# Kernel optimization log

Measured on AMD Instinct MI355X. Metric: run time of the kernel, lower is better.

The kernel has to match this reference:

```python
import jax, jax.numpy as jnp
import numpy as np

B, R, N, K, E = 128, 500, 500, 10, 128
H1 = 5 * E  # UnvisitedMLP hidden = embedding_dim * 5


def setup_inputs() -> dict:
    key = jax.random.key(0)
    ks = jax.random.split(key, 8)
    current = jax.random.randint(ks[0], (B, R), 0, N)
    distance = jax.random.uniform(ks[1], (B, N, N), dtype=jnp.float32)
    # unvisited cities, exercising the padding-index path in search_unvisited.
    visited = jax.random.uniform(ks[2], (B, R, N)) < 0.97
    masked = jnp.where(visited, -jnp.inf, 0.0).astype(jnp.float32)
    encoded_nodes = jax.random.normal(ks[3], (B, N, E), dtype=jnp.float32)
    w1 = jax.random.normal(ks[4], (H1, K * E), dtype=jnp.float32) * (1.0 / np.sqrt(K * E))
    b1 = jnp.zeros((H1,), dtype=jnp.float32)
    w2 = jax.random.normal(ks[5], (E, H1), dtype=jnp.float32) * (1.0 / np.sqrt(H1))
    b2 = jnp.zeros((E,), dtype=jnp.float32)
    return {"current": current, "distance": distance, "masked": masked,
            "encoded_nodes": encoded_nodes, "w1": w1, "b1": b1, "w2": w2, "b2": b2}


def _search_unvisited(current, distance, masked, k_near):
    # distance_filtered[b, r, :] = distance[b, current[b, r], :]  -> [B, R, N]
    b_idx = jnp.arange(current.shape[0])[:, None]
    distance_filtered = distance[b_idx, current, :]
    mask_unvisited = masked != -jnp.inf
    distance_masked = jnp.where(mask_unvisited, distance_filtered, jnp.inf)
    # k smallest == top-k of negated distances
    neg_vals, k_idx = jax.lax.top_k(-distance_masked, k_near)  # [B, R, K]
    is_inf = neg_vals == -jnp.inf  # entries that were +inf (no unvisited left)
    n_cities = distance.shape[1]
    return jnp.where(is_inf, n_cities, k_idx)  # padding index = problem_size


def _gather_pad0(encoded_nodes, idx):
    # pad encoded_nodes with a zero row at index N, then gather  -> [B, R, K, E]
    padded = jnp.concatenate(
        [encoded_nodes, jnp.zeros_like(encoded_nodes[:, :1, :])], axis=1)
    b_idx = jnp.arange(encoded_nodes.shape[0])[:, None, None]
    return padded[b_idx, idx, :]


def _pad_avg(a):
    # replace all-zero (padding) rows along K with the mean of non-zero rows
    is_zero = a.sum(axis=-1) == 0  # [B, R, K]
    nz_count = jnp.clip((~is_zero).sum(axis=-1).astype(jnp.float32), 1e-9)
    mean_vec = a.sum(axis=2) / nz_count[..., None]  # [B, R, E]
    return jnp.where(is_zero[..., None], mean_vec[:, :, None, :], a)


def reference(current, distance, masked, encoded_nodes, w1, b1, w2, b2):
    k_near = K
    idx = _search_unvisited(current, distance, masked, k_near)  # [B, R, K]
    emb = _gather_pad0(encoded_nodes, idx)                      # [B, R, K, E]
    emb = _pad_avg(emb)
    h = emb.reshape(emb.shape[0], emb.shape[1], k_near * emb.shape[-1])  # [B, R, K*E]
    h = jax.nn.relu(jnp.einsum('brf,hf->brh', h, w1) + b1)
    out = jnp.einsum('brh,eh->bre', h, w2) + b2  # [B, R, E]
    return out
```

## Files before the change

kernel.cpp:

```cpp
#include <hip/hip_runtime.h>
#include <cstdint>
#include <cstddef>

#define Bn   128
#define Rn   500
#define Nn   500
#define Kn   10
#define En   128
#define H1n  640
#define KEn  1280
#define Mn   (Bn * Rn)

typedef short s16x8 __attribute__((ext_vector_type(8)));
typedef float f32x4 __attribute__((ext_vector_type(4)));

__device__ __forceinline__ unsigned short f2bf(float x) {
    union { float f; unsigned int u; } v; v.f = x;
    unsigned int r = v.u + 0x7fffu + ((v.u >> 16) & 1u);
    return (unsigned short)(r >> 16);
}
__device__ __forceinline__ float bf2f(unsigned short u) {
    union { unsigned int u; float f; } v; v.u = ((unsigned int)u) << 16;
    return v.f;
}
__device__ __forceinline__ void gl2lds16(const void* g, void* l) {
    __builtin_amdgcn_global_load_lds(
        (const __attribute__((address_space(1))) unsigned int*)g,
        (__attribute__((address_space(3))) unsigned int*)l, 16, 0, 0);
}
__device__ __forceinline__ void drain_all() {
    asm volatile("s_waitcnt vmcnt(0) lgkmcnt(0)" ::: "memory");
}
#define WAITV(n) asm volatile("s_waitcnt vmcnt(" #n ")" ::: "memory")
__device__ __forceinline__ void pipe_barrier() {
    __builtin_amdgcn_s_barrier();
    asm volatile("" ::: "memory");
}

__global__ void convw_kernel(const float* __restrict__ enc, const float* __restrict__ w1,
                             const float* __restrict__ w2,
                             unsigned short* __restrict__ encb, unsigned short* __restrict__ w1b,
                             unsigned short* __restrict__ w2b) {
    int i = blockIdx.x * 256 + threadIdx.x;
    if (i < (Bn * Nn * En) / 4) {
        float4 v = ((const float4*)enc)[i];
        ushort4 o; o.x = f2bf(v.x); o.y = f2bf(v.y); o.z = f2bf(v.z); o.w = f2bf(v.w);
        ((ushort4*)encb)[i] = o;
    }
    if (i < (H1n * KEn) / 4) {
        float4 v = ((const float4*)w1)[i];
        ushort4 o; o.x = f2bf(v.x); o.y = f2bf(v.y); o.z = f2bf(v.z); o.w = f2bf(v.w);
        ((ushort4*)w1b)[i] = o;
    }
    if (i < (En * H1n) / 4) {
        float4 v = ((const float4*)w2)[i];
        ushort4 o; o.x = f2bf(v.x); o.y = f2bf(v.y); o.z = f2bf(v.z); o.w = f2bf(v.w);
        ((ushort4*)w2b)[i] = o;
    }
}

__global__ __launch_bounds__(256) void select_kernel(const int* __restrict__ current,
                            const float* __restrict__ distance,
                            const float* __restrict__ masked,
                            const unsigned short* __restrict__ encb,
                            int* __restrict__ idx_out,
                            unsigned short* __restrict__ meanbb) {
    __shared__ unsigned long long buf[4][512];
    const int wv   = threadIdx.x >> 6;
    const int row  = blockIdx.x * 4 + wv;
    const int lane = threadIdx.x & 63;
    const int b    = row / Rn;
    const int cur  = current[row];
    const uint4* drow4 = (const uint4*)(distance + ((size_t)b * Nn + cur) * Nn);
    const uint4* mrow4 = (const uint4*)(masked + (size_t)row * Nn);
    unsigned long long* wbuf = buf[wv];
    const unsigned long long INFKEY = 0x7F800000FFFFFFFFull;

    uint4 mu[2], du[2];
#pragma unroll
    for (int h = 0; h < 2; ++h) {
        const int c = lane + 64 * h;
        mu[h] = make_uint4(0xFF800000u, 0xFF800000u, 0xFF800000u, 0xFF800000u);
        du[h] = make_uint4(0u, 0u, 0u, 0u);
        if (c < 125) { mu[h] = mrow4[c]; du[h] = drow4[c]; }
    }

    unsigned long long keyr[8];
    unsigned int fm = 0;
#pragma unroll
    for (int h = 0; h < 2; ++h) {
        const unsigned int mm[4] = {mu[h].x, mu[h].y, mu[h].z, mu[h].w};
        const unsigned int dd[4] = {du[h].x, du[h].y, du[h].z, du[h].w};
#pragma unroll
        for (int j = 0; j < 4; ++j) {
            const int e  = h * 4 + j;
            const int nn = 4 * (lane + 64 * h) + j;
            keyr[e] = ((unsigned long long)dd[j] << 32) | (unsigned int)nn;
            fm |= (mm[j] != 0xFF800000u ? 1u : 0u) << e;
        }
    }
    const int lc = __popc(fm);

    int x = lc;
#pragma unroll
    for (int d = 1; d < 64; d <<= 1) {
        const int y = __shfl_up(x, d);
        if (lane >= d) x += y;
    }
    const int n = __shfl(x, 63);
    int off = x - lc;

#pragma unroll
    for (int e = 0; e < 8; ++e) {
        if (fm & (1u << e)) wbuf[off++] = keyr[e];
    }

    int ids[Kn];
    if (n <= 64) {
        unsigned long long key = (lane < n) ? wbuf[lane] : INFKEY;
#pragma unroll
        for (int k = 2; k <= 32; k <<= 1) {
#pragma unroll
            for (int j = k >> 1; j >= 1; j >>= 1) {
                const unsigned long long ok = __shfl_xor(key, j);
                const bool takemin = (((lane & k) == 0) == ((lane & j) == 0));
                const unsigned long long mn = (ok < key) ? ok : key;
                const unsigned long long mx = (ok < key) ? key : ok;
                key = takemin ? mn : mx;
            }
        }
        if (n > 32) {
#pragma unroll
            for (int j = 32; j >= 1; j >>= 1) {
                const unsigned long long ok = __shfl_xor(key, j);
                const bool takemin = (((lane & 64) == 0) == ((lane & j) == 0));
                const unsigned long long mn = (ok < key) ? ok : key;
                const unsigned long long mx = (ok < key) ? key : ok;
                key = takemin ? mn : mx;
            }
        }
        const int wid = ((unsigned int)(key >> 32) >= 0x7F800000u) ? Nn
                                                                   : (int)(key & 0xffffffffu);
        if (lane < Kn) idx_out[row * Kn + lane] = wid;
#pragma unroll
        for (int k = 0; k < Kn; ++k) ids[k] = __shfl(wid, k);
    } else {
        unsigned long long key8[8];
#pragma unroll
        for (int i = 0; i < 8; ++i) {
            const int ii = lane + 64 * i;
            key8[i] = (ii < n) ? wbuf[ii] : INFKEY;
        }
        int myid = Nn;
#pragma unroll
        for (int it = 0; it < Kn; ++it) {
            unsigned long long bk = key8[0];
#pragma unroll
            for (int i = 1; i < 8; ++i) bk = (key8[i] < bk) ? key8[i] : bk;
#pragma unroll
            for (int off2 = 1; off2 < 64; off2 <<= 1) {
                const unsigned long long ok = __shfl_xor(bk, off2);
                bk = (ok < bk) ? ok : bk;
            }
            const int wid = ((unsigned int)(bk >> 32) >= 0x7F800000u) ? Nn
                                                                      : (int)(bk & 0xffffffffu);
            ids[it] = wid;
            if (lane == it) myid = wid;
#pragma unroll
            for (int i = 0; i < 8; ++i)
                if (key8[i] == bk) key8[i] = INFKEY;
        }
        if (lane < Kn) idx_out[row * Kn + lane] = myid;
    }

    const unsigned int* encu = (const unsigned int*)(encb + (size_t)b * Nn * En);
    float s0 = 0.f, s1 = 0.f; int cnt = 0;
#pragma unroll
    for (int k = 0; k < Kn; ++k) {
        const int id = ids[k];
        if (id < Nn) {
            unsigned int u = encu[id * (En / 2) + lane];
            s0 += bf2f((unsigned short)(u & 0xffffu));
            s1 += bf2f((unsigned short)(u >> 16));
            cnt++;
        }
    }
    float m0 = 0.f, m1 = 0.f;
    if (cnt > 0) { m0 = s0 / (float)cnt; m1 = s1 / (float)cnt; }
    unsigned int packed = (unsigned int)f2bf(m0) | ((unsigned int)f2bf(m1) << 16);
    ((unsigned int*)meanbb)[(size_t)row * (En / 2) + lane] = packed;
}

__global__ __launch_bounds__(512, 4) void gemm1_kernel(
        const unsigned short* __restrict__ encb, const unsigned short* __restrict__ meanbb,
        const int* __restrict__ idxb, const unsigned short* __restrict__ w1b,
        const float* __restrict__ b1, unsigned short* __restrict__ hbuf) {
    extern __shared__ unsigned short lds[];
    unsigned short* const As   = lds;
    unsigned short* const Bs   = lds + 3 * 256 * 32;
    unsigned short* const idxs = lds + 3 * 256 * 32 + 3 * 128 * 32;

    const int p  = blockIdx.x;
    const int x  = p & 7;
    const int rk = p >> 3;
    const int w  = (x < 2 ? x * 157 : 314 + (x - 2) * 156) + rk;
    const int row0 = (w / 5) * 256;
    const int h0   = (w % 5) * 128;

    const int t    = threadIdx.x;
    const int lane = t & 63;
    const int wave = t >> 6;
    const int ln15 = lane & 15;
    const int q4   = lane >> 4;
    const int wm4  = wave & 3;
    const int wn   = wave >> 2;

    for (int i = t; i < 256 * Kn; i += 512)
        idxs[i] = (unsigned short)idxb[row0 * Kn + i];

    const int rl   = lane >> 2;
    const int sc   = lane & 3;
    const int coff = (sc ^ ((rl >> 1) & 3)) * 8;

    int lrowA[2];
    const unsigned short* encB[2];
    const unsigned short* meanR[2];
#pragma unroll
    for (int s = 0; s < 2; ++s) {
        lrowA[s] = wave * 32 + s * 16 + rl;
        const int gr = row0 + lrowA[s];
        encB[s]  = encb + (size_t)(gr / Rn) * Nn * En;
        meanR[s] = meanbb + (size_t)gr * En + coff;
    }
    const int lrowB = wave * 16 + rl;
    const unsigned short* w1R = w1b + (size_t)(h0 + lrowB) * KEn + coff;

    f32x4 acc[4][4];
#pragma unroll
    for (int i = 0; i < 4; ++i)
#pragma unroll
        for (int j = 0; j < 4; ++j)
            acc[i][j] = (f32x4){0.f, 0.f, 0.f, 0.f};

    auto issueA = [&](int kt, int cb) {
        const int j  = kt >> 2;
        const int e0 = (kt & 3) * 32;
#pragma unroll
        for (int s = 0; s < 2; ++s) {
            const int id = idxs[lrowA[s] * Kn + j];
            const unsigned short* src = (id < Nn)
                ? (encB[s] + (size_t)id * En + e0 + coff)
                : (meanR[s] + e0);
            gl2lds16(src, As + (size_t)cb * (256 * 32) + (wave * 32 + s * 16) * 32);
        }
    };
    auto issueB = [&](int kt, int cb) {
        gl2lds16(w1R + kt * 32, Bs + (size_t)cb * (128 * 32) + (wave * 16) * 32);
    };

    drain_all();
    __syncthreads();
    issueA(0, 0); issueB(0, 0);
    issueA(1, 1); issueB(1, 1);
    WAITV(3);
    pipe_barrier();

    const int rA  = wm4 * 64 + ln15;
    const int rB  = wn  * 64 + ln15;
    const int slA = (q4 ^ ((rA >> 1) & 3)) * 8;
    const int slB = (q4 ^ ((rB >> 1) & 3)) * 8;

#define MFMA16(a, bvec, c) c = __builtin_amdgcn_mfma_f32_16x16x32_bf16(a, bvec, c, 0, 0, 0)

#pragma unroll
    for (int kt = 0; kt < 40; ++kt) {
        const int cb = kt % 3;
        const unsigned short* Ab = As + cb * (256 * 32);
        const unsigned short* Bb = Bs + cb * (128 * 32);
        s16x8 af0, af1, af2, af3, bq0, bq1;

        af0 = *(const s16x8*)(Ab + (rA +  0) * 32 + slA);
        af1 = *(const s16x8*)(Ab + (rA + 16) * 32 + slA);
        af2 = *(const s16x8*)(Ab + (rA + 32) * 32 + slA);
        af3 = *(const s16x8*)(Ab + (rA + 48) * 32 + slA);
        bq0 = *(const s16x8*)(Bb + (rB +  0) * 32 + slB);
        bq1 = *(const s16x8*)(Bb + (rB + 16) * 32 + slB);
        if (kt + 2 < 40) issueA(kt + 2, (kt + 2) % 3);
        pipe_barrier();
        __builtin_amdgcn_s_setprio(1);
        MFMA16(af0, bq0, acc[0][0]); MFMA16(af1, bq0, acc[1][0]);
        MFMA16(af2, bq0, acc[2][0]); MFMA16(af3, bq0, acc[3][0]);
        MFMA16(af0, bq1, acc[0][1]); MFMA16(af1, bq1, acc[1][1]);
        MFMA16(af2, bq1, acc[2][1]); MFMA16(af3, bq1, acc[3][1]);
        __builtin_amdgcn_s_setprio(0);
        pipe_barrier();

        bq0 = *(const s16x8*)(Bb + (rB + 32) * 32 + slB);
        bq1 = *(const s16x8*)(Bb + (rB + 48) * 32 + slB);
        if (kt + 2 < 40) issueB(kt + 2, (kt + 2) % 3);
        pipe_barrier();
        __builtin_amdgcn_s_setprio(1);
        MFMA16(af0, bq0, acc[0][2]); MFMA16(af1, bq0, acc[1][2]);
        MFMA16(af2, bq0, acc[2][2]); MFMA16(af3, bq0, acc[3][2]);
        MFMA16(af0, bq1, acc[0][3]); MFMA16(af1, bq1, acc[1][3]);
        MFMA16(af2, bq1, acc[2][3]); MFMA16(af3, bq1, acc[3][3]);
        __builtin_amdgcn_s_setprio(0);
        if (kt + 2 < 40)      { WAITV(3); }
        else if (kt + 1 < 40) { WAITV(0); }
        pipe_barrier();
    }
#undef MFMA16

#pragma unroll
    for (int i = 0; i < 4; ++i) {
#pragma unroll
        for (int jj = 0; jj < 4; ++jj) {
            const int h = h0 + wn * 64 + jj * 16 + ln15;
            const float bias = b1[h];
#pragma unroll
            for (int rg = 0; rg < 4; ++rg) {
                const int m = wm4 * 64 + i * 16 + q4 * 4 + rg;
                float vv = acc[i][jj][rg] + bias;
                vv = fmaxf(vv, 0.f);
                hbuf[(size_t)(row0 + m) * H1n + h] = f2bf(vv);
            }
        }
    }
}

__global__ __launch_bounds__(256, 4) void gemm2_kernel(
        const unsigned short* __restrict__ hbuf, const unsigned short* __restrict__ w2b,
        const float* __restrict__ b2, float* __restrict__ out) {
    __shared__ alignas(16) unsigned short As[3][128 * 32];
    __shared__ alignas(16) unsigned short Bs[3][128 * 32];

    const int row0 = blockIdx.x * 128;
    const int t    = threadIdx.x;
    const int lane = t & 63;
    const int wave = t >> 6;
    const int ln15 = lane & 15;
    const int q4   = lane >> 4;
    const int wm   = wave & 1;
    const int wn   = wave >> 1;

    const int rl   = lane >> 2;
    const int sc   = lane & 3;
    const int coff = (sc ^ ((rl >> 1) & 3)) * 8;

    const unsigned short* hrow[2];
    const unsigned short* w2row[2];
#pragma unroll
    for (int s = 0; s < 2; ++s) {
        const int lr = wave * 32 + s * 16 + rl;
        hrow[s]  = hbuf + (size_t)(row0 + lr) * H1n + coff;
        w2row[s] = w2b + (size_t)lr * H1n + coff;
    }

    f32x4 acc[4][4];
#pragma unroll
    for (int i = 0; i < 4; ++i)
#pragma unroll
        for (int j = 0; j < 4; ++j)
            acc[i][j] = (f32x4){0.f, 0.f, 0.f, 0.f};

    auto issueA = [&](int kt, int cb) {
#pragma unroll
        for (int s = 0; s < 2; ++s)
            gl2lds16(hrow[s] + kt * 32, &As[cb][(wave * 32 + s * 16) * 32]);
    };
    auto issueB = [&](int kt, int cb) {
#pragma unroll
        for (int s = 0; s < 2; ++s)
            gl2lds16(w2row[s] + kt * 32, &Bs[cb][(wave * 32 + s * 16) * 32]);
    };

    issueA(0, 0); issueB(0, 0);
    issueA(1, 1); issueB(1, 1);
    WAITV(4);
    pipe_barrier();

    const int rA  = wm * 64 + ln15;
    const int rB  = wn * 64 + ln15;
    const int slA = (q4 ^ ((rA >> 1) & 3)) * 8;
    const int slB = (q4 ^ ((rB >> 1) & 3)) * 8;

#define MFMA16(a, bvec, c) c = __builtin_amdgcn_mfma_f32_16x16x32_bf16(a, bvec, c, 0, 0, 0)

#pragma unroll
    for (int kt = 0; kt < 20; ++kt) {
        const int cb = kt % 3;
        const unsigned short* Ab = As[cb];
        const unsigned short* Bb = Bs[cb];
        s16x8 af0, af1, af2, af3, bq0, bq1;

        af0 = *(const s16x8*)(Ab + (rA +  0) * 32 + slA);
        af1 = *(const s16x8*)(Ab + (rA + 16) * 32 + slA);
        af2 = *(const s16x8*)(Ab + (rA + 32) * 32 + slA);
        af3 = *(const s16x8*)(Ab + (rA + 48) * 32 + slA);
        bq0 = *(const s16x8*)(Bb + (rB +  0) * 32 + slB);
        bq1 = *(const s16x8*)(Bb + (rB + 16) * 32 + slB);
        if (kt + 2 < 20) issueA(kt + 2, (kt + 2) % 3);
        pipe_barrier();
        __builtin_amdgcn_s_setprio(1);
        MFMA16(af0, bq0, acc[0][0]); MFMA16(af1, bq0, acc[1][0]);
        MFMA16(af2, bq0, acc[2][0]); MFMA16(af3, bq0, acc[3][0]);
        MFMA16(af0, bq1, acc[0][1]); MFMA16(af1, bq1, acc[1][1]);
        MFMA16(af2, bq1, acc[2][1]); MFMA16(af3, bq1, acc[3][1]);
        __builtin_amdgcn_s_setprio(0);
        pipe_barrier();

        bq0 = *(const s16x8*)(Bb + (rB + 32) * 32 + slB);
        bq1 = *(const s16x8*)(Bb + (rB + 48) * 32 + slB);
        if (kt + 2 < 20) issueB(kt + 2, (kt + 2) % 3);
        pipe_barrier();
        __builtin_amdgcn_s_setprio(1);
        MFMA16(af0, bq0, acc[0][2]); MFMA16(af1, bq0, acc[1][2]);
        MFMA16(af2, bq0, acc[2][2]); MFMA16(af3, bq0, acc[3][2]);
        MFMA16(af0, bq1, acc[0][3]); MFMA16(af1, bq1, acc[1][3]);
        MFMA16(af2, bq1, acc[2][3]); MFMA16(af3, bq1, acc[3][3]);
        __builtin_amdgcn_s_setprio(0);
        if (kt + 2 < 20)      { WAITV(4); }
        else if (kt + 1 < 20) { WAITV(0); }
        pipe_barrier();
    }
#undef MFMA16

#pragma unroll
    for (int i = 0; i < 4; ++i) {
#pragma unroll
        for (int jj = 0; jj < 4; ++jj) {
            const int e = wn * 64 + jj * 16 + ln15;
            const float bias = b2[e];
#pragma unroll
            for (int rg = 0; rg < 4; ++rg) {
                const int m = wm * 64 + i * 16 + q4 * 4 + rg;
                out[(size_t)(row0 + m) * En + e] = acc[i][jj][rg] + bias;
            }
        }
    }
}

extern "C" void kernel_launch(void* const* d_in, const int* in_sizes, int n_in,
                              void* d_out, int out_size, void* d_ws, size_t ws_size,
                              hipStream_t stream) {
    const int*   current  = (const int*)d_in[0];
    const float* distance = (const float*)d_in[1];
    const float* masked   = (const float*)d_in[2];
    const float* encoded  = (const float*)d_in[3];
    const float* w1       = (const float*)d_in[4];
    const float* b1       = (const float*)d_in[5];
    const float* w2       = (const float*)d_in[6];
    const float* b2       = (const float*)d_in[7];
    float* out = (float*)d_out;

    char* ws = (char*)d_ws;
    const size_t OFF_IDX  = 0;
    const size_t OFF_ENCB = 2560000;
    const size_t OFF_MEAN = OFF_ENCB + 16384000;
    const size_t OFF_W1B  = OFF_MEAN + 16384000;
    const size_t OFF_W2B  = OFF_W1B + 1638400;
    const size_t OFF_H    = OFF_W2B + 163840;
    int*            idxb   = (int*)(ws + OFF_IDX);
    unsigned short* encb   = (unsigned short*)(ws + OFF_ENCB);
    unsigned short* meanbb = (unsigned short*)(ws + OFF_MEAN);
    unsigned short* w1b    = (unsigned short*)(ws + OFF_W1B);
    unsigned short* w2b    = (unsigned short*)(ws + OFF_W2B);
    unsigned short* hbuf   = (unsigned short*)(ws + OFF_H);

    static bool s_attr = false;
    if (!s_attr) {
        hipFuncSetAttribute(reinterpret_cast<const void*>(gemm1_kernel),
                            hipFuncAttributeMaxDynamicSharedMemorySize, 78848);
        s_attr = true;
    }

    convw_kernel<<<(Bn * Nn * En / 4 + 255) / 256, 256, 0, stream>>>(encoded, w1, w2, encb, w1b, w2b);
    select_kernel<<<Mn / 4, 256, 0, stream>>>(current, distance, masked, encb, idxb, meanbb);
    gemm1_kernel<<<1250, 512, 78848, stream>>>(encb, meanbb, idxb, w1b, b1, hbuf);
    gemm2_kernel<<<Mn / 128, 256, 0, stream>>>(hbuf, w2b, b2, out);
}
```

Before: 439.5 us.

## Process four rows per wave in select with prefetch; merge gemm2 k-step phases

The select kernel now has each wave handle four consecutive rows. The next row's distance and mask loads are double-buffered so they overlap the current row's sort and mean work, and the grid shrinks by four. Separately, the gemm2 inner loop loads all four B fragments up front, issues both the A and B async copies together, and runs all 16 MFMAs in a single phase. That drops two pipe barriers per k-step, at the cost of more registers and fewer waves in flight in select.

```diff
diff --git a/kernel.cpp b/kernel.cpp
--- a/kernel.cpp
+++ b/kernel.cpp
@@ -66,129 +66,146 @@
                             int* __restrict__ idx_out,
                             unsigned short* __restrict__ meanbb) {
     __shared__ unsigned long long buf[4][512];
-    const int wv   = threadIdx.x >> 6;
-    const int row  = blockIdx.x * 4 + wv;
-    const int lane = threadIdx.x & 63;
-    const int b    = row / Rn;
-    const int cur  = current[row];
-    const uint4* drow4 = (const uint4*)(distance + ((size_t)b * Nn + cur) * Nn);
-    const uint4* mrow4 = (const uint4*)(masked + (size_t)row * Nn);
+    const int wv    = threadIdx.x >> 6;
+    const int lane  = threadIdx.x & 63;
+    const int rbase = blockIdx.x * 16 + wv * 4;
     unsigned long long* wbuf = buf[wv];
     const unsigned long long INFKEY = 0x7F800000FFFFFFFFull;
 
-    uint4 mu[2], du[2];
-#pragma unroll
-    for (int h = 0; h < 2; ++h) {
-        const int c = lane + 64 * h;
-        mu[h] = make_uint4(0xFF800000u, 0xFF800000u, 0xFF800000u, 0xFF800000u);
-        du[h] = make_uint4(0u, 0u, 0u, 0u);
-        if (c < 125) { mu[h] = mrow4[c]; du[h] = drow4[c]; }
-    }
-
-    unsigned long long keyr[8];
-    unsigned int fm = 0;
-#pragma unroll
-    for (int h = 0; h < 2; ++h) {
-        const unsigned int mm[4] = {mu[h].x, mu[h].y, mu[h].z, mu[h].w};
-        const unsigned int dd[4] = {du[h].x, du[h].y, du[h].z, du[h].w};
-#pragma unroll
-        for (int j = 0; j < 4; ++j) {
-            const int e  = h * 4 + j;
-            const int nn = 4 * (lane + 64 * h) + j;
-            keyr[e] = ((unsigned long long)dd[j] << 32) | (unsigned int)nn;
-            fm |= (mm[j] != 0xFF800000u ? 1u : 0u) << e;
-        }
-    }
-    const int lc = __popc(fm);
-
-    int x = lc;
-#pragma unroll
-    for (int d = 1; d < 64; d <<= 1) {
-        const int y = __shfl_up(x, d);
-        if (lane >= d) x += y;
-    }
-    const int n = __shfl(x, 63);
-    int off = x - lc;
-
-#pragma unroll
-    for (int e = 0; e < 8; ++e) {
-        if (fm & (1u << e)) wbuf[off++] = keyr[e];
-    }
-
-    int ids[Kn];
-    if (n <= 64) {
-        unsigned long long key = (lane < n) ? wbuf[lane] : INFKEY;
-#pragma unroll
-        for (int k = 2; k <= 32; k <<= 1) {
-#pragma unroll
-            for (int j = k >> 1; j >= 1; j >>= 1) {
-                const unsigned long long ok = __shfl_xor(key, j);
-                const bool takemin = (((lane & k) == 0) == ((lane & j) == 0));
-                const unsigned long long mn = (ok < key) ? ok : key;
-                const unsigned long long mx = (ok < key) ? key : ok;
-                key = takemin ? mn : mx;
-            }
-        }
-        if (n > 32) {
-#pragma unroll
-            for (int j = 32; j >= 1; j >>= 1) {
-                const unsigned long long ok = __shfl_xor(key, j);
-                const bool takemin = (((lane & 64) == 0) == ((lane & j) == 0));
-                const unsigned long long mn = (ok < key) ? ok : key;
-                const unsigned long long mx = (ok < key) ? key : ok;
-                key = takemin ? mn : mx;
-            }
-        }
-        const int wid = ((unsigned int)(key >> 32) >= 0x7F800000u) ? Nn
-                                                                   : (int)(key & 0xffffffffu);
-        if (lane < Kn) idx_out[row * Kn + lane] = wid;
-#pragma unroll
-        for (int k = 0; k < Kn; ++k) ids[k] = __shfl(wid, k);
-    } else {
-        unsigned long long key8[8];
-#pragma unroll
-        for (int i = 0; i < 8; ++i) {
-            const int ii = lane + 64 * i;
-            key8[i] = (ii < n) ? wbuf[ii] : INFKEY;
-        }
-        int myid = Nn;
-#pragma unroll
-        for (int it = 0; it < Kn; ++it) {
-            unsigned long long bk = key8[0];
-#pragma unroll
-            for (int i = 1; i < 8; ++i) bk = (key8[i] < bk) ? key8[i] : bk;
-#pragma unroll
-            for (int off2 = 1; off2 < 64; off2 <<= 1) {
-                const unsigned long long ok = __shfl_xor(bk, off2);
-                bk = (ok < bk) ? ok : bk;
-            }
-            const int wid = ((unsigned int)(bk >> 32) >= 0x7F800000u) ? Nn
-                                                                      : (int)(bk & 0xffffffffu);
-            ids[it] = wid;
-            if (lane == it) myid = wid;
-#pragma unroll
-            for (int i = 0; i < 8; ++i)
-                if (key8[i] == bk) key8[i] = INFKEY;
-        }
-        if (lane < Kn) idx_out[row * Kn + lane] = myid;
-    }
-
-    const unsigned int* encu = (const unsigned int*)(encb + (size_t)b * Nn * En);
-    float s0 = 0.f, s1 = 0.f; int cnt = 0;
-#pragma unroll
-    for (int k = 0; k < Kn; ++k) {
-        const int id = ids[k];
-        if (id < Nn) {
-            unsigned int u = encu[id * (En / 2) + lane];
-            s0 += bf2f((unsigned short)(u & 0xffffu));
-            s1 += bf2f((unsigned short)(u >> 16));
-            cnt++;
-        }
-    }
-    float m0 = 0.f, m1 = 0.f;
-    if (cnt > 0) { m0 = s0 / (float)cnt; m1 = s1 / (float)cnt; }
-    unsigned int packed = (unsigned int)f2bf(m0) | ((unsigned int)f2bf(m1) << 16);
-    ((unsigned int*)meanbb)[(size_t)row * (En / 2) + lane] = packed;
+    int curv[4];
+#pragma unroll
+    for (int i = 0; i < 4; ++i) curv[i] = current[rbase + i];
+
+    uint4 mu[2][2], du[2][2];
+
+    auto issue_row = [&](int i, int slot) {
+        const int r   = rbase + i;
+        const int b   = r / Rn;
+        const uint4* drow4 = (const uint4*)(distance + ((size_t)b * Nn + curv[i]) * Nn);
+        const uint4* mrow4 = (const uint4*)(masked + (size_t)r * Nn);
+#pragma unroll
+        for (int h = 0; h < 2; ++h) {
+            const int c = lane + 64 * h;
+            mu[slot][h] = make_uint4(0xFF800000u, 0xFF800000u, 0xFF800000u, 0xFF800000u);
+            du[slot][h] = make_uint4(0u, 0u, 0u, 0u);
+            if (c < 125) { mu[slot][h] = mrow4[c]; du[slot][h] = drow4[c]; }
+        }
+    };
+
+    issue_row(0, 0);
+
+#pragma unroll
+    for (int i = 0; i < 4; ++i) {
+        const int slot = i & 1;
+        if (i + 1 < 4) issue_row(i + 1, slot ^ 1);
+        const int r = rbase + i;
+        const int b = r / Rn;
+
+        unsigned long long keyr[8];
+        unsigned int fm = 0;
+#pragma unroll
+        for (int h = 0; h < 2; ++h) {
+            const unsigned int mm[4] = {mu[slot][h].x, mu[slot][h].y, mu[slot][h].z, mu[slot][h].w};
+            const unsigned int dd[4] = {du[slot][h].x, du[slot][h].y, du[slot][h].z, du[slot][h].w};
+#pragma unroll
+            for (int j = 0; j < 4; ++j) {
+                const int e  = h * 4 + j;
+                const int nn = 4 * (lane + 64 * h) + j;
+                keyr[e] = ((unsigned long long)dd[j] << 32) | (unsigned int)nn;
+                fm |= (mm[j] != 0xFF800000u ? 1u : 0u) << e;
+            }
+        }
+        const int lc = __popc(fm);
+
+        int x = lc;
+#pragma unroll
+        for (int d = 1; d < 64; d <<= 1) {
+            const int y = __shfl_up(x, d);
+            if (lane >= d) x += y;
+        }
+        const int n = __shfl(x, 63);
+        int off = x - lc;
+
+#pragma unroll
+        for (int e = 0; e < 8; ++e) {
+            if (fm & (1u << e)) wbuf[off++] = keyr[e];
+        }
+
+        int ids[Kn];
+        if (n <= 64) {
+            unsigned long long key = (lane < n) ? wbuf[lane] : INFKEY;
+#pragma unroll
+            for (int k = 2; k <= 32; k <<= 1) {
+#pragma unroll
+                for (int j = k >> 1; j >= 1; j >>= 1) {
+                    const unsigned long long ok = __shfl_xor(key, j);
+                    const bool takemin = (((lane & k) == 0) == ((lane & j) == 0));
+                    const unsigned long long mn = (ok < key) ? ok : key;
+                    const unsigned long long mx = (ok < key) ? key : ok;
+                    key = takemin ? mn : mx;
+                }
+            }
+            if (n > 32) {
+#pragma unroll
+                for (int j = 32; j >= 1; j >>= 1) {
+                    const unsigned long long ok = __shfl_xor(key, j);
+                    const bool takemin = (((lane & 64) == 0) == ((lane & j) == 0));
+                    const unsigned long long mn = (ok < key) ? ok : key;
+                    const unsigned long long mx = (ok < key) ? key : ok;
+                    key = takemin ? mn : mx;
+                }
+            }
+            const int wid = ((unsigned int)(key >> 32) >= 0x7F800000u) ? Nn
+                                                                       : (int)(key & 0xffffffffu);
+            if (lane < Kn) idx_out[r * Kn + lane] = wid;
+#pragma unroll
+            for (int k = 0; k < Kn; ++k) ids[k] = __shfl(wid, k);
+        } else {
+            unsigned long long key8[8];
+#pragma unroll
+            for (int q = 0; q < 8; ++q) {
+                const int ii = lane + 64 * q;
+                key8[q] = (ii < n) ? wbuf[ii] : INFKEY;
+            }
+            int myid = Nn;
+#pragma unroll
+            for (int it = 0; it < Kn; ++it) {
+                unsigned long long bk = key8[0];
+#pragma unroll
+                for (int q = 1; q < 8; ++q) bk = (key8[q] < bk) ? key8[q] : bk;
+#pragma unroll
+                for (int off2 = 1; off2 < 64; off2 <<= 1) {
+                    const unsigned long long ok = __shfl_xor(bk, off2);
+                    bk = (ok < bk) ? ok : bk;
+                }
+                const int wid = ((unsigned int)(bk >> 32) >= 0x7F800000u) ? Nn
+                                                                          : (int)(bk & 0xffffffffu);
+                ids[it] = wid;
+                if (lane == it) myid = wid;
+#pragma unroll
+                for (int q = 0; q < 8; ++q)
+                    if (key8[q] == bk) key8[q] = INFKEY;
+            }
+            if (lane < Kn) idx_out[r * Kn + lane] = myid;
+        }
+
+        const unsigned int* encu = (const unsigned int*)(encb + (size_t)b * Nn * En);
+        float s0 = 0.f, s1 = 0.f; int cnt = 0;
+#pragma unroll
+        for (int k = 0; k < Kn; ++k) {
+            const int id = ids[k];
+            if (id < Nn) {
+                unsigned int u = encu[id * (En / 2) + lane];
+                s0 += bf2f((unsigned short)(u & 0xffffu));
+                s1 += bf2f((unsigned short)(u >> 16));
+                cnt++;
+            }
+        }
+        float m0 = 0.f, m1 = 0.f;
+        if (cnt > 0) { m0 = s0 / (float)cnt; m1 = s1 / (float)cnt; }
+        unsigned int packed = (unsigned int)f2bf(m0) | ((unsigned int)f2bf(m1) << 16);
+        ((unsigned int*)meanbb)[(size_t)r * (En / 2) + lane] = packed;
+    }
 }
 
 __global__ __launch_bounds__(512, 4) void gemm1_kernel(
@@ -391,7 +408,7 @@
         const int cb = kt % 3;
         const unsigned short* Ab = As[cb];
         const unsigned short* Bb = Bs[cb];
-        s16x8 af0, af1, af2, af3, bq0, bq1;
+        s16x8 af0, af1, af2, af3, bq0, bq1, bq2, bq3;
 
         af0 = *(const s16x8*)(Ab + (rA +  0) * 32 + slA);
         af1 = *(const s16x8*)(Ab + (rA + 16) * 32 + slA);
@@ -399,25 +416,18 @@
         af3 = *(const s16x8*)(Ab + (rA + 48) * 32 + slA);
         bq0 = *(const s16x8*)(Bb + (rB +  0) * 32 + slB);
         bq1 = *(const s16x8*)(Bb + (rB + 16) * 32 + slB);
-        if (kt + 2 < 20) issueA(kt + 2, (kt + 2) % 3);
-        pipe_barrier();
+        bq2 = *(const s16x8*)(Bb + (rB + 32) * 32 + slB);
+        bq3 = *(const s16x8*)(Bb + (rB + 48) * 32 + slB);
+        if (kt + 2 < 20) { issueA(kt + 2, (kt + 2) % 3); issueB(kt + 2, (kt + 2) % 3); }
         __builtin_amdgcn_s_setprio(1);
         MFMA16(af0, bq0, acc[0][0]); MFMA16(af1, bq0, acc[1][0]);
         MFMA16(af2, bq0, acc[2][0]); MFMA16(af3, bq0, acc[3][0]);
         MFMA16(af0, bq1, acc[0][1]); MFMA16(af1, bq1, acc[1][1]);
         MFMA16(af2, bq1, acc[2][1]); MFMA16(af3, bq1, acc[3][1]);
-        __builtin_amdgcn_s_setprio(0);
-        pipe_barrier();
-
-        bq0 = *(const s16x8*)(Bb + (rB + 32) * 32 + slB);
-        bq1 = *(const s16x8*)(Bb + (rB + 48) * 32 + slB);
-        if (kt + 2 < 20) issueB(kt + 2, (kt + 2) % 3);
-        pipe_barrier();
-        __builtin_amdgcn_s_setprio(1);
-        MFMA16(af0, bq0, acc[0][2]); MFMA16(af1, bq0, acc[1][2]);
-        MFMA16(af2, bq0, acc[2][2]); MFMA16(af3, bq0, acc[3][2]);
-        MFMA16(af0, bq1, acc[0][3]); MFMA16(af1, bq1, acc[1][3]);
-        MFMA16(af2, bq1, acc[2][3]); MFMA16(af3, bq1, acc[3][3]);
+        MFMA16(af0, bq2, acc[0][2]); MFMA16(af1, bq2, acc[1][2]);
+        MFMA16(af2, bq2, acc[2][2]); MFMA16(af3, bq2, acc[3][2]);
+        MFMA16(af0, bq3, acc[0][3]); MFMA16(af1, bq3, acc[1][3]);
+        MFMA16(af2, bq3, acc[2][3]); MFMA16(af3, bq3, acc[3][3]);
         __builtin_amdgcn_s_setprio(0);
         if (kt + 2 < 20)      { WAITV(4); }
         else if (kt + 1 < 20) { WAITV(0); }
@@ -475,7 +485,7 @@
     }
 
     convw_kernel<<<(Bn * Nn * En / 4 + 255) / 256, 256, 0, stream>>>(encoded, w1, w2, encb, w1b, w2b);
-    select_kernel<<<Mn / 4, 256, 0, stream>>>(current, distance, masked, encb, idxb, meanbb);
+    select_kernel<<<Mn / 16, 256, 0, stream>>>(current, distance, masked, encb, idxb, meanbb);
     gemm1_kernel<<<1250, 512, 78848, stream>>>(encb, meanbb, idxb, w1b, b1, hbuf);
     gemm2_kernel<<<Mn / 128, 256, 0, stream>>>(hbuf, w2b, b2, out);
 }
```

Result: slower. 477.4 us (+8.6%).

## Skip mean computation for full rows, precompute gather offsets in registers

Applied to the files above, without the earlier changes.

The select kernel now computes and writes the padding mean only when a row has fewer than K unvisited cities, skipping the gather-and-average for most rows. The first GEMM kernel drops its LDS index table and instead precomputes per-thread 32-bit offsets for all K neighbours (encoded rows or the mean buffer) directly from global memory. This frees LDS and removes a block-wide sync at startup. The second GEMM merges its two half-steps into one with all B fragments loaded up front. Together these cut redundant memory traffic and barriers, at the cost of more registers per thread.

```diff
diff --git a/kernel.cpp b/kernel.cpp
--- a/kernel.cpp
+++ b/kernel.cpp
@@ -115,7 +115,6 @@
         if (fm & (1u << e)) wbuf[off++] = keyr[e];
     }
 
-    int ids[Kn];
     if (n <= 64) {
         unsigned long long key = (lane < n) ? wbuf[lane] : INFKEY;
 #pragma unroll
@@ -142,8 +141,28 @@
         const int wid = ((unsigned int)(key >> 32) >= 0x7F800000u) ? Nn
                                                                    : (int)(key & 0xffffffffu);
         if (lane < Kn) idx_out[row * Kn + lane] = wid;
-#pragma unroll
-        for (int k = 0; k < Kn; ++k) ids[k] = __shfl(wid, k);
+
+        if (n < Kn) {
+            int ids[Kn];
+#pragma unroll
+            for (int k = 0; k < Kn; ++k) ids[k] = __shfl(wid, k);
+            const unsigned int* encu = (const unsigned int*)(encb + (size_t)b * Nn * En);
+            float s0 = 0.f, s1 = 0.f; int cnt = 0;
+#pragma unroll
+            for (int k = 0; k < Kn; ++k) {
+                const int id = ids[k];
+                if (id < Nn) {
+                    unsigned int u = encu[id * (En / 2) + lane];
+                    s0 += bf2f((unsigned short)(u & 0xffffu));
+                    s1 += bf2f((unsigned short)(u >> 16));
+                    cnt++;
+                }
+            }
+            float m0 = 0.f, m1 = 0.f;
+            if (cnt > 0) { m0 = s0 / (float)cnt; m1 = s1 / (float)cnt; }
+            unsigned int packed = (unsigned int)f2bf(m0) | ((unsigned int)f2bf(m1) << 16);
+            ((unsigned int*)meanbb)[(size_t)row * (En / 2) + lane] = packed;
+        }
     } else {
         unsigned long long key8[8];
 #pragma unroll
@@ -164,7 +183,6 @@
             }
             const int wid = ((unsigned int)(bk >> 32) >= 0x7F800000u) ? Nn
                                                                       : (int)(bk & 0xffffffffu);
-            ids[it] = wid;
             if (lane == it) myid = wid;
 #pragma unroll
             for (int i = 0; i < 8; ++i)
@@ -172,23 +190,6 @@
         }
         if (lane < Kn) idx_out[row * Kn + lane] = myid;
     }
-
-    const unsigned int* encu = (const unsigned int*)(encb + (size_t)b * Nn * En);
-    float s0 = 0.f, s1 = 0.f; int cnt = 0;
-#pragma unroll
-    for (int k = 0; k < Kn; ++k) {
-        const int id = ids[k];
-        if (id < Nn) {
-            unsigned int u = encu[id * (En / 2) + lane];
-            s0 += bf2f((unsigned short)(u & 0xffffu));
-            s1 += bf2f((unsigned short)(u >> 16));
-            cnt++;
-        }
-    }
-    float m0 = 0.f, m1 = 0.f;
-    if (cnt > 0) { m0 = s0 / (float)cnt; m1 = s1 / (float)cnt; }
-    unsigned int packed = (unsigned int)f2bf(m0) | ((unsigned int)f2bf(m1) << 16);
-    ((unsigned int*)meanbb)[(size_t)row * (En / 2) + lane] = packed;
 }
 
 __global__ __launch_bounds__(512, 4) void gemm1_kernel(
@@ -196,9 +197,8 @@
         const int* __restrict__ idxb, const unsigned short* __restrict__ w1b,
         const float* __restrict__ b1, unsigned short* __restrict__ hbuf) {
     extern __shared__ unsigned short lds[];
-    unsigned short* const As   = lds;
-    unsigned short* const Bs   = lds + 3 * 256 * 32;
-    unsigned short* const idxs = lds + 3 * 256 * 32 + 3 * 128 * 32;
+    unsigned short* const As = lds;
+    unsigned short* const Bs = lds + 3 * 256 * 32;
 
     const int p  = blockIdx.x;
     const int x  = p & 7;
@@ -215,22 +215,24 @@
     const int wm4  = wave & 3;
     const int wn   = wave >> 2;
 
-    for (int i = t; i < 256 * Kn; i += 512)
-        idxs[i] = (unsigned short)idxb[row0 * Kn + i];
-
     const int rl   = lane >> 2;
     const int sc   = lane & 3;
     const int coff = (sc ^ ((rl >> 1) & 3)) * 8;
 
+    const unsigned int MEANOFF = 8192000u;
+    unsigned int offA[2][Kn];
     int lrowA[2];
-    const unsigned short* encB[2];
-    const unsigned short* meanR[2];
 #pragma unroll
     for (int s = 0; s < 2; ++s) {
         lrowA[s] = wave * 32 + s * 16 + rl;
         const int gr = row0 + lrowA[s];
-        encB[s]  = encb + (size_t)(gr / Rn) * Nn * En;
-        meanR[s] = meanbb + (size_t)gr * En + coff;
+        const unsigned int encbase  = (unsigned int)((gr / Rn) * (Nn * En)) + (unsigned int)coff;
+        const unsigned int meanbase = MEANOFF + (unsigned int)gr * En + (unsigned int)coff;
+#pragma unroll
+        for (int j = 0; j < Kn; ++j) {
+            const int id = idxb[gr * Kn + j];
+            offA[s][j] = (id < Nn) ? (encbase + (unsigned int)id * En) : meanbase;
+        }
     }
     const int lrowB = wave * 16 + rl;
     const unsigned short* w1R = w1b + (size_t)(h0 + lrowB) * KEn + coff;
@@ -246,20 +248,15 @@
         const int j  = kt >> 2;
         const int e0 = (kt & 3) * 32;
 #pragma unroll
-        for (int s = 0; s < 2; ++s) {
-            const int id = idxs[lrowA[s] * Kn + j];
-            const unsigned short* src = (id < Nn)
-                ? (encB[s] + (size_t)id * En + e0 + coff)
-                : (meanR[s] + e0);
-            gl2lds16(src, As + (size_t)cb * (256 * 32) + (wave * 32 + s * 16) * 32);
-        }
+        for (int s = 0; s < 2; ++s)
+            gl2lds16(encb + offA[s][j] + e0,
+                     As + (size_t)cb * (256 * 32) + (wave * 32 + s * 16) * 32);
     };
     auto issueB = [&](int kt, int cb) {
         gl2lds16(w1R + kt * 32, Bs + (size_t)cb * (128 * 32) + (wave * 16) * 32);
     };
 
-    drain_all();
-    __syncthreads();
+    WAITV(0);
     issueA(0, 0); issueB(0, 0);
     issueA(1, 1); issueB(1, 1);
     WAITV(3);
@@ -391,7 +388,7 @@
         const int cb = kt % 3;
         const unsigned short* Ab = As[cb];
         const unsigned short* Bb = Bs[cb];
-        s16x8 af0, af1, af2, af3, bq0, bq1;
+        s16x8 af0, af1, af2, af3, bq0, bq1, bq2, bq3;
 
         af0 = *(const s16x8*)(Ab + (rA +  0) * 32 + slA);
         af1 = *(const s16x8*)(Ab + (rA + 16) * 32 + slA);
@@ -399,25 +396,18 @@
         af3 = *(const s16x8*)(Ab + (rA + 48) * 32 + slA);
         bq0 = *(const s16x8*)(Bb + (rB +  0) * 32 + slB);
         bq1 = *(const s16x8*)(Bb + (rB + 16) * 32 + slB);
-        if (kt + 2 < 20) issueA(kt + 2, (kt + 2) % 3);
-        pipe_barrier();
+        bq2 = *(const s16x8*)(Bb + (rB + 32) * 32 + slB);
+        bq3 = *(const s16x8*)(Bb + (rB + 48) * 32 + slB);
+        if (kt + 2 < 20) { issueA(kt + 2, (kt + 2) % 3); issueB(kt + 2, (kt + 2) % 3); }
         __builtin_amdgcn_s_setprio(1);
         MFMA16(af0, bq0, acc[0][0]); MFMA16(af1, bq0, acc[1][0]);
         MFMA16(af2, bq0, acc[2][0]); MFMA16(af3, bq0, acc[3][0]);
         MFMA16(af0, bq1, acc[0][1]); MFMA16(af1, bq1, acc[1][1]);
         MFMA16(af2, bq1, acc[2][1]); MFMA16(af3, bq1, acc[3][1]);
-        __builtin_amdgcn_s_setprio(0);
-        pipe_barrier();
-
-        bq0 = *(const s16x8*)(Bb + (rB + 32) * 32 + slB);
-        bq1 = *(const s16x8*)(Bb + (rB + 48) * 32 + slB);
-        if (kt + 2 < 20) issueB(kt + 2, (kt + 2) % 3);
-        pipe_barrier();
-        __builtin_amdgcn_s_setprio(1);
-        MFMA16(af0, bq0, acc[0][2]); MFMA16(af1, bq0, acc[1][2]);
-        MFMA16(af2, bq0, acc[2][2]); MFMA16(af3, bq0, acc[3][2]);
-        MFMA16(af0, bq1, acc[0][3]); MFMA16(af1, bq1, acc[1][3]);
-        MFMA16(af2, bq1, acc[2][3]); MFMA16(af3, bq1, acc[3][3]);
+        MFMA16(af0, bq2, acc[0][2]); MFMA16(af1, bq2, acc[1][2]);
+        MFMA16(af2, bq2, acc[2][2]); MFMA16(af3, bq2, acc[3][2]);
+        MFMA16(af0, bq3, acc[0][3]); MFMA16(af1, bq3, acc[1][3]);
+        MFMA16(af2, bq3, acc[2][3]); MFMA16(af3, bq3, acc[3][3]);
         __builtin_amdgcn_s_setprio(0);
         if (kt + 2 < 20)      { WAITV(4); }
         else if (kt + 1 < 20) { WAITV(0); }
@@ -470,12 +460,12 @@
     static bool s_attr = false;
     if (!s_attr) {
         hipFuncSetAttribute(reinterpret_cast<const void*>(gemm1_kernel),
-                            hipFuncAttributeMaxDynamicSharedMemorySize, 78848);
+                            hipFuncAttributeMaxDynamicSharedMemorySize, 73728);
         s_attr = true;
     }
 
     convw_kernel<<<(Bn * Nn * En / 4 + 255) / 256, 256, 0, stream>>>(encoded, w1, w2, encb, w1b, w2b);
     select_kernel<<<Mn / 4, 256, 0, stream>>>(current, distance, masked, encb, idxb, meanbb);
-    gemm1_kernel<<<1250, 512, 78848, stream>>>(encb, meanbb, idxb, w1b, b1, hbuf);
+    gemm1_kernel<<<1250, 512, 73728, stream>>>(encb, meanbb, idxb, w1b, b1, hbuf);
     gemm2_kernel<<<Mn / 128, 256, 0, stream>>>(hbuf, w2b, b2, out);
 }
```

Measured after the change: 423.1 us. 1.04x faster.
